# Optimization experiments

Measured on AMD Instinct MI355X. Metric: run time of the kernel, lower is better.

Reference implementation:

```python
import jax, jax.numpy as jnp
import numpy as np
import math

B, S, D, H, F = 2, 2048, 1024, 16, 4096
HD = D // H
EPS = 1e-5

def _alibi_slopes(n_heads):
    # n_heads is a power of 2 here (16): m_i = start * start**i, start = 2^(-2^(-(log2(n)-3)))
    start = 2.0 ** (-(2.0 ** (-(math.log2(n_heads) - 3))))
    return np.array([start * (start ** i) for i in range(n_heads)], dtype=np.float32)

SLOPES = jnp.asarray(_alibi_slopes(H))  # (H,)


def setup_inputs() -> dict:
    key = jax.random.key(0)
    ks = jax.random.split(key, 8)
    s = 0.02
    return {
        "x":  jax.random.normal(ks[0], (B, S, D), jnp.float32),
        "Wq": jax.random.normal(ks[1], (D, D), jnp.float32) * s,
        "Wk": jax.random.normal(ks[2], (D, D), jnp.float32) * s,
        "Wv": jax.random.normal(ks[3], (D, D), jnp.float32) * s,
        "Wo": jax.random.normal(ks[4], (D, D), jnp.float32) * s,
        "bo": jnp.zeros((D,), jnp.float32),
        "W1": jax.random.normal(ks[5], (F, D), jnp.float32) * s,
        "b1": jnp.zeros((F,), jnp.float32),
        "W2": jax.random.normal(ks[6], (D, F), jnp.float32) * s,
        "b2": jnp.zeros((D,), jnp.float32),
        "g1": jnp.ones((D,), jnp.float32),
        "be1": jnp.zeros((D,), jnp.float32),
        "g2": jnp.ones((D,), jnp.float32),
        "be2": jnp.zeros((D,), jnp.float32),
    }


def _layernorm(h, g, b):
    mu = jnp.mean(h, axis=-1, keepdims=True)
    var = jnp.mean((h - mu) ** 2, axis=-1, keepdims=True)
    return (h - mu) * jax.lax.rsqrt(var + EPS) * g + b


def reference(x, Wq, Wk, Wv, Wo, bo, W1, b1, W2, b2, g1, be1, g2, be2):
    # --- pre-norm ALiBi attention ---
    h = _layernorm(x, g1, be1)
    q = (h @ Wq.T).reshape(B, S, H, HD).transpose(0, 2, 1, 3)  # (B,H,S,HD)
    k = (h @ Wk.T).reshape(B, S, H, HD).transpose(0, 2, 1, 3)
    v = (h @ Wv.T).reshape(B, S, H, HD).transpose(0, 2, 1, 3)
    scores = jnp.einsum("bhqd,bhkd->bhqk", q, k) / math.sqrt(HD)
    pos = jnp.arange(S)
    dist = (pos[None, :] - pos[:, None]).astype(jnp.float32)      # (S,S): j - i
    bias = SLOPES[:, None, None] * dist[None, :, :]               # (H,S,S)
    attn = jax.nn.softmax(scores + bias[None], axis=-1)
    ao = jnp.einsum("bhqk,bhkd->bhqd", attn, v)
    ao = ao.transpose(0, 2, 1, 3).reshape(B, S, D) @ Wo.T + bo
    x = x + ao
    # --- pre-norm FFN ---
    h2 = _layernorm(x, g2, be2)
    ff = jax.nn.relu(h2 @ W1.T + b1) @ W2.T + b2
    return x + ff
```

## Files before the change

### kernel.cpp

```cpp
#include <hip/hip_runtime.h>
#include <hip/hip_bf16.h>
#include <stdint.h>

typedef unsigned short u16;
typedef __attribute__((ext_vector_type(8))) short short8;
typedef __attribute__((ext_vector_type(4))) float f32x4;

#define S_LEN 2048
#define D_DIM 1024
#define NHEAD 16
#define HDIM 64
#define NROWS 4096

__device__ __forceinline__ u16 f2bf(float f) {
  union { float f; uint32_t u; } c; c.f = f;
  uint32_t r = (c.u + 0x7fffu + ((c.u >> 16) & 1u)) >> 16;
  return (u16)r;
}

__device__ __forceinline__ float bf2f(u16 v) {
  union { uint32_t u; float f; } c; c.u = ((uint32_t)v) << 16;
  return c.f;
}

__device__ __forceinline__ uint32_t pack_bf2(float a, float b) {
  __hip_bfloat162 h = __float22bfloat162_rn(float2{a, b});
  union { __hip_bfloat162 h; uint32_t u; } c; c.h = h;
  return c.u;
}

__device__ __forceinline__ void gload_lds16(const void* g, void* l) {
  typedef const __attribute__((address_space(1))) unsigned int gq_t;
  typedef __attribute__((address_space(3))) unsigned int lq_t;
  __builtin_amdgcn_global_load_lds((gq_t*)(uintptr_t)g,
                                   (lq_t*)(uint32_t)(uintptr_t)l, 16, 0, 0);
}

__global__ __launch_bounds__(256) void cast_all(const float* __restrict__ Wq,
                                                const float* __restrict__ Wk,
                                                const float* __restrict__ Wv,
                                                const float* __restrict__ Wo,
                                                const float* __restrict__ W1,
                                                const float* __restrict__ W2,
                                                u16* __restrict__ wqkv,
                                                u16* __restrict__ wo,
                                                u16* __restrict__ w1,
                                                u16* __restrict__ w2) {
  int i = blockIdx.x * 256 + threadIdx.x;
  const float* src;
  u16* dst;
  int rel;
  if (i < 786432) {
    int ws = i / 262144;
    rel = i - ws * 262144;
    src = (ws == 0) ? Wq : ((ws == 1) ? Wk : Wv);
    dst = wqkv + (size_t)ws * 1048576;
  } else if (i < 1048576) {
    rel = i - 786432; src = Wo; dst = wo;
  } else if (i < 2097152) {
    rel = i - 1048576; src = W1; dst = w1;
  } else {
    rel = i - 2097152; src = W2; dst = w2;
  }
  float4 v = ((const float4*)src)[rel];
  ((ushort4*)dst)[rel] = make_ushort4(f2bf(v.x), f2bf(v.y), f2bf(v.z), f2bf(v.w));
}

__global__ __launch_bounds__(256) void ln_kernel(const float* __restrict__ x,
                                                 const float* __restrict__ g,
                                                 const float* __restrict__ be,
                                                 u16* __restrict__ out) {
  int row = blockIdx.x;
  int tid = threadIdx.x;
  const float4 v = ((const float4*)(x + (size_t)row * D_DIM))[tid];
  float s = v.x + v.y + v.z + v.w;
  float s2 = v.x * v.x + v.y * v.y + v.z * v.z + v.w * v.w;
#pragma unroll
  for (int off = 1; off < 64; off <<= 1) {
    s += __shfl_xor(s, off);
    s2 += __shfl_xor(s2, off);
  }
  __shared__ float ss[4], ss2[4];
  if ((tid & 63) == 0) { ss[tid >> 6] = s; ss2[tid >> 6] = s2; }
  __syncthreads();
  s = ss[0] + ss[1] + ss[2] + ss[3];
  s2 = ss2[0] + ss2[1] + ss2[2] + ss2[3];
  float mu = s * (1.0f / D_DIM);
  float var = s2 * (1.0f / D_DIM) - mu * mu;
  float rs = rsqrtf(var + 1e-5f);
  float4 gv = ((const float4*)g)[tid];
  float4 bv = ((const float4*)be)[tid];
  ushort4 o = make_ushort4(f2bf((v.x - mu) * rs * gv.x + bv.x),
                           f2bf((v.y - mu) * rs * gv.y + bv.y),
                           f2bf((v.z - mu) * rs * gv.z + bv.z),
                           f2bf((v.w - mu) * rs * gv.w + bv.w));
  ((ushort4*)(out + (size_t)row * D_DIM))[tid] = o;
}

template <int EPI>
__global__ __launch_bounds__(512, 2) void gemm8p(const u16* __restrict__ A,
                                                 const u16* __restrict__ Bw,
                                                 void* __restrict__ Cout,
                                                 const float* __restrict__ bias,
                                                 int M, int N, int K, int ksl) {
  __shared__ char L0[131072];
  const int tid = threadIdx.x;
  const int wid = tid >> 6, lane = tid & 63;
  const int l4 = lane & 15, lh = lane >> 4;
  const int wr = wid >> 2, wc = wid & 3;
  const int nbn = N >> 8;
  const int nwg = (M >> 8) * nbn;
  const int slice = blockIdx.x / nwg;
  const int id0 = blockIdx.x % nwg;
  const int t0 = (id0 & 7) * (nwg >> 3) + (id0 >> 3);
  const int bm = t0 / nbn, bn = t0 % nbn;
  const int Ks = K / ksl;
  const int NG = Ks >> 6;

  f32x4 acc[8][4];
#pragma unroll
  for (int i = 0; i < 8; ++i)
#pragma unroll
    for (int j = 0; j < 4; ++j) acc[i][j] = (f32x4){0.f, 0.f, 0.f, 0.f};

  const int srow4 = lane >> 2;
  const int sblk = (lane & 3) ^ ((lane >> 3) & 3);
  const u16* Asrc = A + ((size_t)(bm * 256 + wid * 16 + srow4)) * K + (size_t)slice * Ks + sblk * 8;
  const u16* Bsrc = Bw + ((size_t)(bn * 256 + wid * 16 + srow4)) * K + (size_t)slice * Ks + sblk * 8;
  const size_t hstr = (size_t)128 * K;
#define STG(MAT, SRC, H, KT, TB)                                             \
  {                                                                          \
    const u16* s_ = (SRC) + (size_t)(H) * hstr + (KT) * 64;                  \
    char* d_ = L0 + (TB) * 65536 + (MAT) * 32768 + ((H) * 128 + wid * 16) * 64; \
    gload_lds16(s_, d_);                                                     \
    gload_lds16(s_ + 32, d_ + 16384);                                        \
  }

  const int swz = (lh ^ ((l4 >> 1) & 3)) << 4;
  const int aB = (wr * 128 + l4) * 64 + swz;
  const int bB = 32768 + (wc * 64 + l4) * 64 + swz;
#define RDA(LC, M_, KS) (*(const short8*)((LC) + (KS)*16384 + (M_)*1024 + aB))
#define RDB(LC, N_, KS) (*(const short8*)((LC) + (KS)*16384 + (N_)*1024 + bB))

  STG(0, Asrc, 0, 0, 0); STG(0, Asrc, 1, 0, 0);
  STG(1, Bsrc, 0, 0, 0); STG(1, Bsrc, 1, 0, 0);
  STG(1, Bsrc, 0, 1, 1); STG(1, Bsrc, 1, 1, 1);
  asm volatile("s_waitcnt vmcnt(4)" ::: "memory");
  __builtin_amdgcn_s_barrier();

  for (int g = 0; g < NG; ++g) {
    const char* Lc = L0 + (g & 1) * 65536;
    const int tbo = (g + 1) & 1;
    short8 aF[4][2], aG[4][2], bF[2][2], bG[2][2];

#pragma unroll
    for (int m = 0; m < 4; ++m) { aF[m][0] = RDA(Lc, m, 0); aF[m][1] = RDA(Lc, m, 1); }
#pragma unroll
    for (int n = 0; n < 2; ++n) { bF[n][0] = RDB(Lc, n, 0); bF[n][1] = RDB(Lc, n, 1); }
    if (g + 1 < NG) STG(0, Asrc, 0, g + 1, tbo);
    __builtin_amdgcn_s_barrier();
    asm volatile("s_waitcnt lgkmcnt(0)" ::: "memory");
    __builtin_amdgcn_sched_barrier(0);
    __builtin_amdgcn_s_setprio(1);
#pragma unroll
    for (int m = 0; m < 4; ++m)
#pragma unroll
      for (int n = 0; n < 2; ++n) {
        acc[m][n] = __builtin_amdgcn_mfma_f32_16x16x32_bf16(aF[m][0], bF[n][0], acc[m][n], 0, 0, 0);
        acc[m][n] = __builtin_amdgcn_mfma_f32_16x16x32_bf16(aF[m][1], bF[n][1], acc[m][n], 0, 0, 0);
      }
    __builtin_amdgcn_s_setprio(0);
    __builtin_amdgcn_s_barrier();

#pragma unroll
    for (int n = 0; n < 2; ++n) { bG[n][0] = RDB(Lc, n + 2, 0); bG[n][1] = RDB(Lc, n + 2, 1); }
    if (g + 1 < NG) STG(0, Asrc, 1, g + 1, tbo);
    __builtin_amdgcn_s_barrier();
    asm volatile("s_waitcnt lgkmcnt(0)" ::: "memory");
    __builtin_amdgcn_sched_barrier(0);
    __builtin_amdgcn_s_setprio(1);
#pragma unroll
    for (int m = 0; m < 4; ++m)
#pragma unroll
      for (int n = 0; n < 2; ++n) {
        acc[m][n + 2] = __builtin_amdgcn_mfma_f32_16x16x32_bf16(aF[m][0], bG[n][0], acc[m][n + 2], 0, 0, 0);
        acc[m][n + 2] = __builtin_amdgcn_mfma_f32_16x16x32_bf16(aF[m][1], bG[n][1], acc[m][n + 2], 0, 0, 0);
      }
    __builtin_amdgcn_s_setprio(0);
    __builtin_amdgcn_s_barrier();

#pragma unroll
    for (int m = 0; m < 4; ++m) { aG[m][0] = RDA(Lc, m + 4, 0); aG[m][1] = RDA(Lc, m + 4, 1); }
    if (g + 2 < NG) STG(1, Bsrc, 0, g + 2, (g & 1));
    __builtin_amdgcn_s_barrier();
    asm volatile("s_waitcnt lgkmcnt(0)" ::: "memory");
    __builtin_amdgcn_sched_barrier(0);
    __builtin_amdgcn_s_setprio(1);
#pragma unroll
    for (int m = 0; m < 4; ++m)
#pragma unroll
      for (int n = 0; n < 2; ++n) {
        acc[m + 4][n] = __builtin_amdgcn_mfma_f32_16x16x32_bf16(aG[m][0], bF[n][0], acc[m + 4][n], 0, 0, 0);
        acc[m + 4][n] = __builtin_amdgcn_mfma_f32_16x16x32_bf16(aG[m][1], bF[n][1], acc[m + 4][n], 0, 0, 0);
      }
    __builtin_amdgcn_s_setprio(0);
    __builtin_amdgcn_s_barrier();

    if (g + 2 < NG) STG(1, Bsrc, 1, g + 2, (g & 1));
    __builtin_amdgcn_s_setprio(1);
#pragma unroll
    for (int m = 0; m < 4; ++m)
#pragma unroll
      for (int n = 0; n < 2; ++n) {
        acc[m + 4][n + 2] = __builtin_amdgcn_mfma_f32_16x16x32_bf16(aG[m][0], bG[n][0], acc[m + 4][n + 2], 0, 0, 0);
        acc[m + 4][n + 2] = __builtin_amdgcn_mfma_f32_16x16x32_bf16(aG[m][1], bG[n][1], acc[m + 4][n + 2], 0, 0, 0);
      }
    __builtin_amdgcn_s_setprio(0);
    if (g + 1 < NG) {
      if (g + 2 < NG) {
        asm volatile("s_waitcnt vmcnt(4)" ::: "memory");
      } else {
        asm volatile("s_waitcnt vmcnt(0)" ::: "memory");
      }
      __builtin_amdgcn_s_barrier();
    }
  }

  const int row0 = bm * 256 + wr * 128 + lh * 4;
  const int col0 = bn * 256 + wc * 64 + l4;
  u16* Cp = (u16*)Cout + (size_t)slice * M * N;
#pragma unroll
  for (int m = 0; m < 8; ++m) {
#pragma unroll
    for (int n = 0; n < 4; ++n) {
      int col = col0 + n * 16;
#pragma unroll
      for (int r = 0; r < 4; ++r) {
        size_t idx = (size_t)(row0 + m * 16 + r) * N + col;
        float v = acc[m][n][r];
        if (EPI == 0) {
          ((u16*)Cout)[idx] = f2bf(v);
        } else if (EPI == 2) {
          v += bias[col];
          ((u16*)Cout)[idx] = f2bf(v > 0.f ? v : 0.f);
        } else {
          Cp[idx] = f2bf(v);
        }
      }
    }
  }
#undef STG
#undef RDA
#undef RDB
}

template <int EPI>
__global__ __launch_bounds__(256) void gemm_bt(const u16* __restrict__ A,
                                               const u16* __restrict__ Bw,
                                               void* __restrict__ Cout,
                                               const float* __restrict__ bias,
                                               const float* __restrict__ resid,
                                               int M, int N, int K, int ksl) {
  __shared__ u16 lsA[128 * 64];
  __shared__ u16 lsB[128 * 64];
  const int tid = threadIdx.x;
  const int wid = tid >> 6, lane = tid & 63;
  const int l4 = lane & 15, lh = lane >> 4;
  const int nbn = N >> 7;
  const int nwgs = (M >> 7) * nbn;
  const int slice = blockIdx.x / nwgs;
  const int id0 = blockIdx.x % nwgs;
  const int t = (id0 & 7) * (nwgs >> 3) + (id0 >> 3);
  const int bm = t / nbn, bn = t % nbn;
  const int wr = wid >> 1, wc = wid & 1;
  const int Ks = K / ksl;

  f32x4 acc[4][4];
#pragma unroll
  for (int i = 0; i < 4; ++i)
#pragma unroll
    for (int j = 0; j < 4; ++j) acc[i][j] = (f32x4){0.f, 0.f, 0.f, 0.f};

  const u16* Ab = A + (size_t)bm * 128 * K + (size_t)slice * Ks;
  const u16* Bb = Bw + (size_t)bn * 128 * K + (size_t)slice * Ks;
  const int srow = (lane >> 3);
  const int scol = (lane & 7) * 8;

  for (int k0 = 0; k0 < Ks; k0 += 64) {
#pragma unroll
    for (int c = 0; c < 4; ++c) {
      int ch = wid * 4 + c;
      int row = ch * 8 + srow;
      gload_lds16(Ab + (size_t)row * K + k0 + scol, &lsA[ch * 512]);
      gload_lds16(Bb + (size_t)row * K + k0 + scol, &lsB[ch * 512]);
    }
    __syncthreads();
#pragma unroll
    for (int ks = 0; ks < 2; ++ks) {
      short8 af[4], bf[4];
#pragma unroll
      for (int i = 0; i < 4; ++i) {
        af[i] = *(const short8*)&lsA[(wr * 64 + i * 16 + l4) * 64 + ks * 32 + lh * 8];
        bf[i] = *(const short8*)&lsB[(wc * 64 + i * 16 + l4) * 64 + ks * 32 + lh * 8];
      }
#pragma unroll
      for (int i = 0; i < 4; ++i)
#pragma unroll
        for (int j = 0; j < 4; ++j)
          acc[i][j] = __builtin_amdgcn_mfma_f32_16x16x32_bf16(af[i], bf[j], acc[i][j], 0, 0, 0);
    }
    __syncthreads();
  }

  const int row0 = bm * 128 + wr * 64;
  const int col0 = bn * 128 + wc * 64;
  float* Cp = (float*)Cout + (size_t)slice * M * N;
#pragma unroll
  for (int i = 0; i < 4; ++i) {
#pragma unroll
    for (int j = 0; j < 4; ++j) {
      int col = col0 + j * 16 + l4;
#pragma unroll
      for (int r = 0; r < 4; ++r) {
        int row = row0 + i * 16 + lh * 4 + r;
        size_t idx = (size_t)row * N + col;
        float v = acc[i][j][r];
        if (EPI == 1) {
          ((float*)Cout)[idx] = v + bias[col] + resid[idx];
        } else {
          Cp[idx] = v;
        }
      }
    }
  }
}

__global__ __launch_bounds__(256) void reduce4_kernel(const u16* __restrict__ pk,
                                                      const float* __restrict__ resid,
                                                      const float* __restrict__ bias,
                                                      float* __restrict__ out) {
  const size_t SL = (size_t)NROWS * D_DIM;
  int i = blockIdx.x * 256 + threadIdx.x;
  short8 p0 = *(const short8*)(pk + (size_t)i * 8);
  short8 p1 = *(const short8*)(pk + SL + (size_t)i * 8);
  short8 p2 = *(const short8*)(pk + 2 * SL + (size_t)i * 8);
  short8 p3 = *(const short8*)(pk + 3 * SL + (size_t)i * 8);
  int col = (i * 8) & (D_DIM - 1);
  float4 b0 = *(const float4*)(bias + col);
  float4 b1 = *(const float4*)(bias + col + 4);
  float4 r0 = ((const float4*)resid)[i * 2];
  float4 r1 = ((const float4*)resid)[i * 2 + 1];
  float o[8];
#pragma unroll
  for (int j = 0; j < 8; ++j)
    o[j] = bf2f((u16)p0[j]) + bf2f((u16)p1[j]) + bf2f((u16)p2[j]) + bf2f((u16)p3[j]);
  float4 w0 = {o[0] + b0.x + r0.x, o[1] + b0.y + r0.y, o[2] + b0.z + r0.z, o[3] + b0.w + r0.w};
  float4 w1 = {o[4] + b1.x + r1.x, o[5] + b1.y + r1.y, o[6] + b1.z + r1.z, o[7] + b1.w + r1.w};
  ((float4*)out)[i * 2] = w0;
  ((float4*)out)[i * 2 + 1] = w1;
}

__global__ __launch_bounds__(256) void transpose_v(const u16* __restrict__ qkv,
                                                   u16* __restrict__ vt) {
  const int gw = blockIdx.x * 4 + (threadIdx.x >> 6);
  const int lane = threadIdx.x & 63;
  const int bh = gw >> 5;
  const int st = gw & 31;
  const int b = bh >> 4, h = bh & 15;
  const u16* src = qkv + (size_t)(b * S_LEN + st * 64) * 3072 + 2048 + h * 64 + lane;
  short8 acc8[8];
#pragma unroll
  for (int o = 0; o < 8; ++o)
#pragma unroll
    for (int i = 0; i < 8; ++i)
      acc8[o][i] = (short)src[(size_t)(o * 8 + i) * 3072];
  u16* dst = vt + ((size_t)bh * 64 + lane) * S_LEN + st * 64;
#pragma unroll
  for (int o = 0; o < 8; ++o) *(short8*)(dst + o * 8) = acc8[o];
}

__global__ __launch_bounds__(256, 4) void attn_kernel(const u16* __restrict__ qkv,
                                                      const u16* __restrict__ vt,
                                                      u16* __restrict__ ao,
                                                      float* __restrict__ pO,
                                                      float* __restrict__ pML) {
  const int id = blockIdx.x;
  const int sub = id & 63;
  const int ugrp = id >> 6;
  int h, j;
  if (ugrp < 15) { h = 15 - ugrp / 3; j = ugrp % 3; }
  else if (ugrp < 19) { h = 10 - ((ugrp - 15) >> 1); j = (ugrp - 15) & 1; }
  else { h = 27 - ugrp; j = 0; }
  const int b = sub >> 5, qt = sub & 31;
  const int bh = b * 16 + h;
  const int tid = threadIdx.x;
  const int wid = tid >> 6, lane = tid & 63;
  const int l4 = lane & 15, lh = lane >> 4;

  __shared__ u16 Kt[2][64 * 64];
  __shared__ u16 Vt[2][64 * 64];
  __shared__ u16 Pt[4][16 * 64];

  const size_t RS = 3 * D_DIM;
  const u16* base = qkv + (size_t)b * S_LEN * RS + h * HDIM;
  const u16* kbase = base + D_DIM;
  const u16* vtb = vt + (size_t)bh * HDIM * S_LEN;
  char* PtW = (char*)Pt[wid];

  short8 qf[2];
  {
    const u16* qp = base + (size_t)(qt * 64 + wid * 16 + l4) * RS + lh * 8;
    qf[0] = *(const short8*)qp;
    qf[1] = *(const short8*)(qp + 32);
  }

  int koff[4][2];
#pragma unroll
  for (int nb = 0; nb < 4; ++nb)
#pragma unroll
    for (int ks = 0; ks < 2; ++ks) {
      int row = nb * 16 + l4;
      koff[nb][ks] = row * 128 + (((ks * 32 + lh * 8) * 2) ^ ((row & 7) << 4));
    }
  int poff[2];
#pragma unroll
  for (int ks = 0; ks < 2; ++ks)
    poff[ks] = l4 * 128 + (((ks * 64 + lh * 16)) ^ ((l4 & 7) << 4));
  int pwoff[4];
#pragma unroll
  for (int nb = 0; nb < 4; ++nb)
    pwoff[nb] = l4 * 128 + (((lh * 8 + nb * 32)) ^ ((l4 & 7) << 4));

  const float slope2 = exp2f(-0.5f * (float)(h + 1)) * 1.44269504088896f;
  const float scale2 = 0.125f * 1.44269504088896f;
  const int ibase = lh * 4 - (qt * 64 + wid * 16 + l4);
  float bc[4][4];
#pragma unroll
  for (int nb = 0; nb < 4; ++nb)
#pragma unroll
    for (int r = 0; r < 4; ++r)
      bc[nb][r] = slope2 * (float)(ibase + 16 * nb + r);

  int nt = (int)ceilf(40.0f / (64.0f * slope2)) + 1;
  if (nt > 32) nt = 32;
  const int nsp = (nt + 11) / 12;
  const int ktmin = 32 - nt;
  const int hi = 31 - j * 12;
  int lo = hi - 11;
  if (lo < ktmin) lo = ktmin;

  float m = -1e30f;
  f32x4 lacc = (f32x4){0.f, 0.f, 0.f, 0.f};
  f32x4 accO[4];
#pragma unroll
  for (int nd = 0; nd < 4; ++nd) accO[nd] = (f32x4){0.f, 0.f, 0.f, 0.f};
  const short8 vones = {(short)0x3F80, (short)0x3F80, (short)0x3F80, (short)0x3F80,
                        (short)0x3F80, (short)0x3F80, (short)0x3F80, (short)0x3F80};

  const int srow = tid >> 3;
  const int sc8 = (tid & 7) * 8;
  const int swo = srow * 128 + ((sc8 * 2) ^ ((srow & 7) << 4));
  short8 kreg[2], vreg[2];
#define STAGE_LOAD(KT)                                                              \
  {                                                                                 \
    kreg[0] = *(const short8*)(kbase + (size_t)((KT)*64 + srow) * RS + sc8);        \
    kreg[1] = *(const short8*)(kbase + (size_t)((KT)*64 + srow + 32) * RS + sc8);   \
    vreg[0] = *(const short8*)(vtb + (size_t)srow * S_LEN + (KT)*64 + sc8);         \
    vreg[1] = *(const short8*)(vtb + (size_t)(srow + 32) * S_LEN + (KT)*64 + sc8);  \
  }
#define STAGE_WRITE(B)                                   \
  {                                                      \
    *(short8*)((char*)Kt[B] + swo) = kreg[0];            \
    *(short8*)((char*)Kt[B] + swo + 4096) = kreg[1];     \
    *(short8*)((char*)Vt[B] + swo) = vreg[0];            \
    *(short8*)((char*)Vt[B] + swo + 4096) = vreg[1];     \
  }

  STAGE_LOAD(hi);
  STAGE_WRITE(0);
  __syncthreads();
  int cur = 0;
  float ktoff = slope2 * 64.0f * (float)hi;
  const float dko = slope2 * 64.0f;

  for (int kt = hi; kt >= lo; --kt) {
    if (kt > lo) STAGE_LOAD(kt - 1);
    const char* Kc = (const char*)Kt[cur];
    const char* Vc = (const char*)Vt[cur];

    f32x4 sacc[4];
#pragma unroll
    for (int nb = 0; nb < 4; ++nb) sacc[nb] = (f32x4){0.f, 0.f, 0.f, 0.f};
    __builtin_amdgcn_s_setprio(1);
#pragma unroll
    for (int ks = 0; ks < 2; ++ks)
#pragma unroll
      for (int nb = 0; nb < 4; ++nb) {
        short8 kf = *(const short8*)(Kc + koff[nb][ks]);
        sacc[nb] = __builtin_amdgcn_mfma_f32_16x16x32_bf16(kf, qf[ks], sacc[nb], 0, 0, 0);
      }
    __builtin_amdgcn_s_setprio(0);

    float p[4][4];
#pragma unroll
    for (int nb = 0; nb < 4; ++nb)
#pragma unroll
      for (int r = 0; r < 4; ++r)
        p[nb][r] = fmaf(sacc[nb][r], scale2, bc[nb][r]);

    float mx0 = fmaxf(fmaxf(p[0][0], p[0][1]), fmaxf(p[0][2], p[0][3]));
    float mx1 = fmaxf(fmaxf(p[1][0], p[1][1]), fmaxf(p[1][2], p[1][3]));
    float mx2 = fmaxf(fmaxf(p[2][0], p[2][1]), fmaxf(p[2][2], p[2][3]));
    float mx3 = fmaxf(fmaxf(p[3][0], p[3][1]), fmaxf(p[3][2], p[3][3]));
    float tm = fmaxf(fmaxf(mx0, mx1), fmaxf(mx2, mx3));
    tm = fmaxf(tm, __shfl_xor(tm, 16));
    tm = fmaxf(tm, __shfl_xor(tm, 32));

    float mm = m - ktoff;
    if (__any(tm > mm)) {
      float mn = fmaxf(mm, tm);
      float corr = exp2f(mm - mn);
      m = mn + ktoff;
      mm = mn;
      float cb[4];
#pragma unroll
      for (int r = 0; r < 4; ++r)
        cb[r] = __shfl(corr, (lane & 48) | (lh * 4 + r));
#pragma unroll
      for (int nd = 0; nd < 4; ++nd)
#pragma unroll
        for (int r = 0; r < 4; ++r) accO[nd][r] *= cb[r];
#pragma unroll
      for (int r = 0; r < 4; ++r) lacc[r] *= cb[r];
    }

#pragma unroll
    for (int nb = 0; nb < 4; ++nb)
#pragma unroll
      for (int r = 0; r < 4; ++r) p[nb][r] = exp2f(p[nb][r] - mm);

#pragma unroll
    for (int nb = 0; nb < 4; ++nb) {
      uint32_t w0 = pack_bf2(p[nb][0], p[nb][1]);
      uint32_t w1 = pack_bf2(p[nb][2], p[nb][3]);
      *(uint2*)(PtW + pwoff[nb]) = make_uint2(w0, w1);
    }
    asm volatile("s_waitcnt lgkmcnt(0)" ::: "memory");

    __builtin_amdgcn_s_setprio(1);
#pragma unroll
    for (int ks = 0; ks < 2; ++ks) {
      short8 pf = *(const short8*)(PtW + poff[ks]);
      lacc = __builtin_amdgcn_mfma_f32_16x16x32_bf16(pf, vones, lacc, 0, 0, 0);
#pragma unroll
      for (int nd = 0; nd < 4; ++nd) {
        short8 vf = *(const short8*)(Vc + koff[nd][ks]);
        accO[nd] = __builtin_amdgcn_mfma_f32_16x16x32_bf16(pf, vf, accO[nd], 0, 0, 0);
      }
    }
    __builtin_amdgcn_s_setprio(0);

    if (kt > lo) STAGE_WRITE(cur ^ 1);
    __syncthreads();
    cur ^= 1;
    ktoff -= dko;
  }

  if (nsp == 1) {
    float ib[4];
#pragma unroll
    for (int r = 0; r < 4; ++r) ib[r] = 1.0f / lacc[r];
    u16* aop = ao + ((size_t)(b * S_LEN + qt * 64 + wid * 16 + lh * 4)) * D_DIM + h * HDIM;
#pragma unroll
    for (int nd = 0; nd < 4; ++nd)
#pragma unroll
      for (int r = 0; r < 4; ++r)
        aop[(size_t)r * D_DIM + nd * 16 + l4] = f2bf(accO[nd][r] * ib[r]);
  } else {
    const int sbase = (h <= 10) ? (h - 9) * 2 : 4 + (h - 11) * 3;
    const int pidx = sub * 19 + sbase + j;
    float* Op = pO + (size_t)pidx * 4096;
#pragma unroll
    for (int nd = 0; nd < 4; ++nd)
#pragma unroll
      for (int r = 0; r < 4; ++r)
        Op[(wid * 16 + lh * 4 + r) * 64 + nd * 16 + l4] = accO[nd][r];
    float mq[4];
#pragma unroll
    for (int r = 0; r < 4; ++r)
      mq[r] = __shfl(m, (lane & 48) | (lh * 4 + r));
    if (l4 == 0) {
      float* mlp = pML + (size_t)pidx * 128 + (wid * 16 + lh * 4) * 2;
#pragma unroll
      for (int r = 0; r < 4; ++r) {
        mlp[r * 2] = mq[r];
        mlp[r * 2 + 1] = lacc[r];
      }
    }
  }
#undef STAGE_LOAD
#undef STAGE_WRITE
}

__global__ __launch_bounds__(256) void attn_combine(const float* __restrict__ pO,
                                                    const float* __restrict__ pML,
                                                    u16* __restrict__ ao) {
  const int g = blockIdx.x;
  const int sub = g & 63;
  const int h = 9 + (g >> 6);
  const int b = sub >> 5, qt = sub & 31;
  const int nsp = (h <= 10) ? 2 : 3;
  const int sbase = (h <= 10) ? (h - 9) * 2 : 4 + (h - 11) * 3;
  const int pidx0 = sub * 19 + sbase;
  const int tid = threadIdx.x;
  const int row = tid >> 2;
  const int d0 = (tid & 3) * 16;

  float mj[3], lj[3];
#pragma unroll
  for (int k = 0; k < 3; ++k) { mj[k] = -1e30f; lj[k] = 0.f; }
  for (int k = 0; k < nsp; ++k) {
    mj[k] = pML[(size_t)(pidx0 + k) * 128 + row * 2];
    lj[k] = pML[(size_t)(pidx0 + k) * 128 + row * 2 + 1];
  }
  float ms = fmaxf(mj[0], fmaxf(mj[1], mj[2]));
  float w[3];
  float lsum = 0.f;
#pragma unroll
  for (int k = 0; k < 3; ++k) {
    w[k] = exp2f(mj[k] - ms);
    lsum += w[k] * lj[k];
  }
  float inv = 1.0f / lsum;

  u16* aop = ao + ((size_t)(b * S_LEN + qt * 64 + row)) * D_DIM + h * HDIM + d0;
#pragma unroll
  for (int c = 0; c < 4; ++c) {
    float4 o = {0.f, 0.f, 0.f, 0.f};
    for (int k = 0; k < nsp; ++k) {
      const float4 v = *(const float4*)(pO + (size_t)(pidx0 + k) * 4096 + row * 64 + d0 + c * 4);
      o.x += w[k] * v.x; o.y += w[k] * v.y; o.z += w[k] * v.z; o.w += w[k] * v.w;
    }
    ushort4 u4 = make_ushort4(f2bf(o.x * inv), f2bf(o.y * inv), f2bf(o.z * inv), f2bf(o.w * inv));
    *(ushort4*)(aop + c * 4) = u4;
  }
}

extern "C" void kernel_launch(void* const* d_in, const int* in_sizes, int n_in,
                              void* d_out, int out_size, void* d_ws, size_t ws_size,
                              hipStream_t stream) {
  const float* x   = (const float*)d_in[0];
  const float* Wq  = (const float*)d_in[1];
  const float* Wk  = (const float*)d_in[2];
  const float* Wv  = (const float*)d_in[3];
  const float* Wo  = (const float*)d_in[4];
  const float* bo  = (const float*)d_in[5];
  const float* W1  = (const float*)d_in[6];
  const float* b1  = (const float*)d_in[7];
  const float* W2  = (const float*)d_in[8];
  const float* b2  = (const float*)d_in[9];
  const float* g1  = (const float*)d_in[10];
  const float* be1 = (const float*)d_in[11];
  const float* g2  = (const float*)d_in[12];
  const float* be2 = (const float*)d_in[13];

  char* p = (char*)d_ws;
  u16* wqkv = (u16*)p; p += (size_t)3072 * 1024 * 2;
  u16* wo   = (u16*)p; p += (size_t)1024 * 1024 * 2;
  u16* w1   = (u16*)p; p += (size_t)4096 * 1024 * 2;
  u16* w2   = (u16*)p; p += (size_t)4096 * 1024 * 2;
  u16* hb   = (u16*)p; p += (size_t)4096 * 1024 * 2;
  u16* qkvb = (u16*)p; p += (size_t)4096 * 3072 * 2;
  u16* aob  = (u16*)p; p += (size_t)4096 * 1024 * 2;
  float* x1 = (float*)p; p += (size_t)4096 * 1024 * 4;
  u16* h2b  = (u16*)p; p += (size_t)4096 * 1024 * 2;
  u16* ff1  = (u16*)p; p += (size_t)4096 * 4096 * 2;
  u16* vt   = ff1;
  float* pO = (float*)(ff1 + (size_t)4 * 1024 * 1024);
  float* pML = pO + (size_t)1216 * 4096;
  u16* pk = hb;

  cast_all<<<12288, 256, 0, stream>>>(Wq, Wk, Wv, Wo, W1, W2, wqkv, wo, w1, w2);

  ln_kernel<<<4096, 256, 0, stream>>>(x, g1, be1, hb);
  gemm8p<0><<<16 * 12, 512, 0, stream>>>(hb, wqkv, qkvb, nullptr, 4096, 3072, 1024, 1);
  transpose_v<<<256, 256, 0, stream>>>(qkvb, vt);
  attn_kernel<<<1792, 256, 0, stream>>>(qkvb, vt, aob, pO, pML);
  attn_combine<<<448, 256, 0, stream>>>(pO, pML, aob);
  gemm_bt<1><<<32 * 8, 256, 0, stream>>>(aob, wo, x1, bo, x, 4096, 1024, 1024, 1);
  ln_kernel<<<4096, 256, 0, stream>>>(x1, g2, be2, h2b);
  gemm8p<2><<<16 * 16, 512, 0, stream>>>(h2b, w1, ff1, b1, 4096, 4096, 1024, 1);
  gemm8p<3><<<4 * 64, 512, 0, stream>>>(ff1, w2, pk, nullptr, 4096, 1024, 4096, 4);
  reduce4_kernel<<<2048, 256, 0, stream>>>(pk, x1, b2, (float*)d_out);
}
```

Baseline: 223.8 us.

## Fuse V transpose into QKV GEMM epilogue, swizzle gemm_bt LDS, drop sched barriers

The QKV GEMM gets a new epilogue mode that writes the V columns straight into the transposed per-head layout, so the separate transpose_v kernel and its extra pass over V are removed. The gemm_bt kernel gets an XOR swizzle on its LDS rows to cut bank conflicts on the fragment reads. Three sched_barrier hints in the main gemm8p loop are also removed, leaving instruction ordering to the compiler. The transposed V stores are strided scatters, one element per lane, which may be poorly coalesced, and dropping the sched barriers can change how MFMA and LDS work interleave.

Measured after the change: 239.0 us. +6.8%, slower.

```diff
diff --git a/kernel.cpp b/kernel.cpp
--- a/kernel.cpp
+++ b/kernel.cpp
@@ -102,6 +102,7 @@
                                                  const u16* __restrict__ Bw,
                                                  void* __restrict__ Cout,
                                                  const float* __restrict__ bias,
+                                                 u16* __restrict__ vt2,
                                                  int M, int N, int K, int ksl) {
   __shared__ char L0[131072];
   const int tid = threadIdx.x;
@@ -160,7 +161,6 @@
     if (g + 1 < NG) STG(0, Asrc, 0, g + 1, tbo);
     __builtin_amdgcn_s_barrier();
     asm volatile("s_waitcnt lgkmcnt(0)" ::: "memory");
-    __builtin_amdgcn_sched_barrier(0);
     __builtin_amdgcn_s_setprio(1);
 #pragma unroll
     for (int m = 0; m < 4; ++m)
@@ -177,7 +177,6 @@
     if (g + 1 < NG) STG(0, Asrc, 1, g + 1, tbo);
     __builtin_amdgcn_s_barrier();
     asm volatile("s_waitcnt lgkmcnt(0)" ::: "memory");
-    __builtin_amdgcn_sched_barrier(0);
     __builtin_amdgcn_s_setprio(1);
 #pragma unroll
     for (int m = 0; m < 4; ++m)
@@ -194,7 +193,6 @@
     if (g + 2 < NG) STG(1, Bsrc, 0, g + 2, (g & 1));
     __builtin_amdgcn_s_barrier();
     asm volatile("s_waitcnt lgkmcnt(0)" ::: "memory");
-    __builtin_amdgcn_sched_barrier(0);
     __builtin_amdgcn_s_setprio(1);
 #pragma unroll
     for (int m = 0; m < 4; ++m)
@@ -236,15 +234,24 @@
       int col = col0 + n * 16;
 #pragma unroll
       for (int r = 0; r < 4; ++r) {
-        size_t idx = (size_t)(row0 + m * 16 + r) * N + col;
+        int row = row0 + m * 16 + r;
+        size_t idx = (size_t)row * N + col;
         float v = acc[m][n][r];
         if (EPI == 0) {
           ((u16*)Cout)[idx] = f2bf(v);
         } else if (EPI == 2) {
           v += bias[col];
           ((u16*)Cout)[idx] = f2bf(v > 0.f ? v : 0.f);
+        } else if (EPI == 3) {
+          Cp[idx] = f2bf(v);
         } else {
-          Cp[idx] = f2bf(v);
+          if (col < 2048) {
+            ((u16*)Cout)[idx] = f2bf(v);
+          } else {
+            int hd = col - 2048;
+            size_t vidx = ((size_t)((row >> 11) * 16 + (hd >> 6)) * 64 + (hd & 63)) * 2048 + (row & 2047);
+            vt2[vidx] = f2bf(v);
+          }
         }
       }
     }
@@ -284,7 +291,7 @@
   const u16* Ab = A + (size_t)bm * 128 * K + (size_t)slice * Ks;
   const u16* Bb = Bw + (size_t)bn * 128 * K + (size_t)slice * Ks;
   const int srow = (lane >> 3);
-  const int scol = (lane & 7) * 8;
+  const int scol = ((lane & 7) ^ srow) * 8;
 
   for (int k0 = 0; k0 < Ks; k0 += 64) {
 #pragma unroll
@@ -300,8 +307,9 @@
       short8 af[4], bf[4];
 #pragma unroll
       for (int i = 0; i < 4; ++i) {
-        af[i] = *(const short8*)&lsA[(wr * 64 + i * 16 + l4) * 64 + ks * 32 + lh * 8];
-        bf[i] = *(const short8*)&lsB[(wc * 64 + i * 16 + l4) * 64 + ks * 32 + lh * 8];
+        int blk = ((ks * 4 + lh) ^ (l4 & 7)) * 8;
+        af[i] = *(const short8*)&lsA[(wr * 64 + i * 16 + l4) * 64 + blk];
+        bf[i] = *(const short8*)&lsB[(wc * 64 + i * 16 + l4) * 64 + blk];
       }
 #pragma unroll
       for (int i = 0; i < 4; ++i)
@@ -358,25 +366,6 @@
   float4 w1 = {o[4] + b1.x + r1.x, o[5] + b1.y + r1.y, o[6] + b1.z + r1.z, o[7] + b1.w + r1.w};
   ((float4*)out)[i * 2] = w0;
   ((float4*)out)[i * 2 + 1] = w1;
-}
-
-__global__ __launch_bounds__(256) void transpose_v(const u16* __restrict__ qkv,
-                                                   u16* __restrict__ vt) {
-  const int gw = blockIdx.x * 4 + (threadIdx.x >> 6);
-  const int lane = threadIdx.x & 63;
-  const int bh = gw >> 5;
-  const int st = gw & 31;
-  const int b = bh >> 4, h = bh & 15;
-  const u16* src = qkv + (size_t)(b * S_LEN + st * 64) * 3072 + 2048 + h * 64 + lane;
-  short8 acc8[8];
-#pragma unroll
-  for (int o = 0; o < 8; ++o)
-#pragma unroll
-    for (int i = 0; i < 8; ++i)
-      acc8[o][i] = (short)src[(size_t)(o * 8 + i) * 3072];
-  u16* dst = vt + ((size_t)bh * 64 + lane) * S_LEN + st * 64;
-#pragma unroll
-  for (int o = 0; o < 8; ++o) *(short8*)(dst + o * 8) = acc8[o];
 }
 
 __global__ __launch_bounds__(256, 4) void attn_kernel(const u16* __restrict__ qkv,
@@ -683,13 +672,12 @@
   cast_all<<<12288, 256, 0, stream>>>(Wq, Wk, Wv, Wo, W1, W2, wqkv, wo, w1, w2);
 
   ln_kernel<<<4096, 256, 0, stream>>>(x, g1, be1, hb);
-  gemm8p<0><<<16 * 12, 512, 0, stream>>>(hb, wqkv, qkvb, nullptr, 4096, 3072, 1024, 1);
-  transpose_v<<<256, 256, 0, stream>>>(qkvb, vt);
+  gemm8p<4><<<16 * 12, 512, 0, stream>>>(hb, wqkv, qkvb, nullptr, vt, 4096, 3072, 1024, 1);
   attn_kernel<<<1792, 256, 0, stream>>>(qkvb, vt, aob, pO, pML);
   attn_combine<<<448, 256, 0, stream>>>(pO, pML, aob);
   gemm_bt<1><<<32 * 8, 256, 0, stream>>>(aob, wo, x1, bo, x, 4096, 1024, 1024, 1);
   ln_kernel<<<4096, 256, 0, stream>>>(x1, g2, be2, h2b);
-  gemm8p<2><<<16 * 16, 512, 0, stream>>>(h2b, w1, ff1, b1, 4096, 4096, 1024, 1);
-  gemm8p<3><<<4 * 64, 512, 0, stream>>>(ff1, w2, pk, nullptr, 4096, 1024, 4096, 4);
+  gemm8p<2><<<16 * 16, 512, 0, stream>>>(h2b, w1, ff1, b1, nullptr, 4096, 4096, 1024, 1);
+  gemm8p<3><<<4 * 64, 512, 0, stream>>>(ff1, w2, pk, nullptr, nullptr, 4096, 1024, 4096, 4);
   reduce4_kernel<<<2048, 256, 0, stream>>>(pk, x1, b2, (float*)d_out);
 }
```
